# Kernel optimization log

Measured on AMD Instinct MI355X. Metric: run time of the kernel, lower is better.

The kernel has to match this reference:

```python
import jax, jax.numpy as jnp
import numpy as np

NUM_NEIGHBORS = 3
EPS = 1e-10
B, N1, N2 = 8, 8192, 2048
C1, C2 = 256, 512


def setup_inputs() -> dict:
    key = jax.random.key(0)
    k1, k2, k3, k4 = jax.random.split(key, 4)
    return {
        "query_xyz": jax.random.uniform(k1, (B, 3, N1), dtype=jnp.float32),
        "key_xyz": jax.random.uniform(k2, (B, 3, N2), dtype=jnp.float32),
        "query_feature": jax.random.normal(k3, (B, C1, N1), dtype=jnp.float32),
        "key_feature": jax.random.normal(k4, (B, C2, N2), dtype=jnp.float32),
    }


def reference(query_xyz, key_xyz, query_feature, key_feature):
    # q: (B, N1, 3), k: (B, N2, 3)
    q = jnp.swapaxes(query_xyz, 1, 2)
    k = jnp.swapaxes(key_xyz, 1, 2)
    # squared pairwise distances (B, N1, N2) via ||q||^2 + ||k||^2 - 2 q.k
    d2 = (
        jnp.sum(q * q, axis=-1, keepdims=True)
        + jnp.sum(k * k, axis=-1)[:, None, :]
        - 2.0 * jnp.einsum("bnd,bmd->bnm", q, k)
    )
    # k nearest neighbors (smallest distances)
    neg_d, index = jax.lax.top_k(-d2, NUM_NEIGHBORS)  # (B, N1, K)
    distance = jnp.maximum(-neg_d, EPS)
    inv_distance = 1.0 / distance
    weight = inv_distance / jnp.sum(inv_distance, axis=2, keepdims=True)
    # torch.no_grad() block -> constants w.r.t. autodiff
    weight = jax.lax.stop_gradient(weight)
    index = jax.lax.stop_gradient(index)
    # gather key features: feat_t (B, N2, C2) -> gathered (B, N1, K, C2)
    feat_t = jnp.swapaxes(key_feature, 1, 2)
    batch_idx = jnp.arange(feat_t.shape[0])[:, None, None]
    gathered = feat_t[batch_idx, index]
    # inverse-distance weighted sum -> (B, C2, N1)
    interpolated = jnp.einsum("bnk,bnkc->bcn", weight, gathered)
    return jnp.concatenate([interpolated, query_feature], axis=1)
```

## Files before the change

kernel.cpp:

```cpp
#include <hip/hip_runtime.h>

#define NB 8
#define N1 8192
#define N2 2048
#define C1 256
#define C2 512
#define CO 768
#define CCH 4


#define NRM2(X, Y, Z) ({                                                   \
    float _s, _t;                                                          \
    asm("v_mul_f32 %0, %2, %2\n\t"                                         \
        "v_mul_f32 %1, %3, %3\n\t"                                         \
        "v_add_f32 %0, %0, %1\n\t"                                         \
        "v_mul_f32 %1, %4, %4\n\t"                                         \
        "v_add_f32 %0, %0, %1"                                             \
        : "=&v"(_s), "=&v"(_t) : "v"(X), "v"(Y), "v"(Z));                  \
    _s; })

#define D2PIN(QX, QY, QZ, QQ, X, Y, Z, KK) ({                              \
    float _d, _t;                                                          \
    asm("v_mul_f32 %0, %2, %5\n\t"             \
        "v_fma_f32 %0, %3, %6, %0\n\t"         \
        "v_fma_f32 %0, %4, %7, %0\n\t"         \
        "v_add_f32 %1, %8, %9\n\t"             \
        "v_mul_f32 %0, 2.0, %0\n\t"            \
        "v_sub_f32 %0, %1, %0"                 \
        : "=&v"(_d), "=&v"(_t)                                             \
        : "v"(QX), "v"(QY), "v"(QZ), "v"(X), "v"(Y), "v"(Z),               \
          "v"(QQ), "v"(KK));                                               \
    _d; })

__global__ __launch_bounds__(256, 4) void knn_fused(
    const float* __restrict__ qxyz,
    const float* __restrict__ kxyz,
    int*   __restrict__ nn_idx,
    float* __restrict__ nn_w)
{
    __shared__ __align__(16) float skx[N2];
    __shared__ __align__(16) float sky[N2];
    __shared__ __align__(16) float skz[N2];
    __shared__ __align__(16) float skk[N2];
    __shared__ float pd[4][64][3];
    __shared__ int   pi[4][64][3];

    const int b   = blockIdx.x >> 7;
    const int n0  = (blockIdx.x & 127) * 64;
    const int tid = threadIdx.x;
    const int w   = tid >> 6, lane = tid & 63;

    const float* kb = kxyz + (size_t)b * 3 * N2;
    for (int j = tid; j < N2; j += 256) {
        float x = kb[j], y = kb[N2 + j], z = kb[2 * N2 + j];
        skx[j] = x; sky[j] = y; skz[j] = z;
        skk[j] = NRM2(x, y, z);
    }
    __syncthreads();

    const int n = n0 + lane;
    const float* qb = qxyz + (size_t)b * 3 * N1;
    const float qx = qb[n], qy = qb[N1 + n], qz = qb[2 * N1 + n];
    const float qq = NRM2(qx, qy, qz);

    float b0 = 3.4e38f, b1 = 3.4e38f, b2 = 3.4e38f;
    int   i0 = 0, i1 = 0, i2 = 0;

#define PROC(X, Y, Z, KK, J) do {                                          \
        float d2 = D2PIN(qx, qy, qz, qq, (X), (Y), (Z), (KK));             \
        if (d2 < b2) {                                                     \
            bool c0 = d2 < b0, c1 = d2 < b1;                               \
            b2 = c1 ? b1 : d2;               i2 = c1 ? i1 : (J);           \
            b1 = c0 ? b0 : (c1 ? d2 : b1);   i1 = c0 ? i0 : (c1 ? (J) : i1); \
            b0 = c0 ? d2 : b0;               i0 = c0 ? (J) : i0;           \
        }                                                                  \
    } while (0)

    const int jlo = w * (N2 / 4), jhi = jlo + (N2 / 4);
    #pragma unroll 4
    for (int jb = jlo; jb < jhi; jb += 4) {
        float4 x4 = *(const float4*)&skx[jb];
        float4 y4 = *(const float4*)&sky[jb];
        float4 z4 = *(const float4*)&skz[jb];
        float4 k4 = *(const float4*)&skk[jb];
        PROC(x4.x, y4.x, z4.x, k4.x, jb + 0);
        PROC(x4.y, y4.y, z4.y, k4.y, jb + 1);
        PROC(x4.z, y4.z, z4.z, k4.z, jb + 2);
        PROC(x4.w, y4.w, z4.w, k4.w, jb + 3);
    }
#undef PROC

    pd[w][lane][0] = b0; pd[w][lane][1] = b1; pd[w][lane][2] = b2;
    pi[w][lane][0] = i0; pi[w][lane][1] = i1; pi[w][lane][2] = i2;
    __syncthreads();

    if (tid < 64) {
        float m0 = 3.4e38f, m1 = 3.4e38f, m2 = 3.4e38f;
        int   j0 = 0, j1 = 0, j2 = 0;
        #pragma unroll
        for (int c = 0; c < 4; ++c) {
            #pragma unroll
            for (int s = 0; s < 3; ++s) {
                float d = pd[c][tid][s];
                int   i = pi[c][tid][s];
                if (d < m2) {
                    bool c0 = d < m0, c1 = d < m1;
                    m2 = c1 ? m1 : d;                j2 = c1 ? j1 : i;
                    m1 = c0 ? m0 : (c1 ? d : m1);    j1 = c0 ? j0 : (c1 ? i : j1);
                    m0 = c0 ? d : m0;                j0 = c0 ? i  : j0;
                }
            }
        }
        float d0f = fmaxf(m0, 1e-10f), d1f = fmaxf(m1, 1e-10f), d2f = fmaxf(m2, 1e-10f);
        float v0 = __fdiv_rn(1.0f, d0f), v1 = __fdiv_rn(1.0f, d1f), v2 = __fdiv_rn(1.0f, d2f);
        float s  = __fadd_rn(__fadd_rn(v0, v1), v2);
        const size_t p = ((size_t)b * N1 + n0 + tid) * 3;
        nn_idx[p] = j0; nn_idx[p + 1] = j1; nn_idx[p + 2] = j2;
        nn_w[p]   = __fdiv_rn(v0, s);
        nn_w[p+1] = __fdiv_rn(v1, s);
        nn_w[p+2] = __fdiv_rn(v2, s);
    }
}

__global__ __launch_bounds__(256) void interp3(
    const float* __restrict__ kfeat,
    const int*   __restrict__ nn_idx,
    const float* __restrict__ nn_w,
    float* __restrict__ out)
{
    __shared__ float skf[N2 * 5];
    const int b     = blockIdx.x & 7;
    const int cg    = blockIdx.x >> 3;
    const int cbase = cg * CCH;
    const int tid   = threadIdx.x;

    const float* kf = kfeat + (size_t)b * C2 * N2 + (size_t)cbase * N2;
    for (int idx = tid; idx < CCH * N2; idx += 256) {
        int c = idx >> 11, j = idx & (N2 - 1);
        skf[j * 5 + c] = kf[(size_t)c * N2 + j];
    }
    __syncthreads();

    const int*   ib = nn_idx + (size_t)b * N1 * 3;
    const float* wb = nn_w   + (size_t)b * N1 * 3;
    float* ob = out + (size_t)b * CO * N1;

    #pragma unroll 4
    for (int t = 0; t < N1 / 256; ++t) {
        const int n = t * 256 + tid;
        const int   i0 = ib[n * 3], i1 = ib[n * 3 + 1], i2 = ib[n * 3 + 2];
        const float w0 = wb[n * 3], w1 = wb[n * 3 + 1], w2 = wb[n * 3 + 2];
        #pragma unroll
        for (int c = 0; c < CCH; ++c) {
            float f0 = skf[i0 * 5 + c], f1 = skf[i1 * 5 + c], f2 = skf[i2 * 5 + c];
            ob[(size_t)(cbase + c) * N1 + n] =
                fmaf(w2, f2, fmaf(w1, f1, __fmul_rn(w0, f0)));
        }
    }
}

__global__ __launch_bounds__(256) void copy_kernel(
    const float* __restrict__ qfeat,
    float* __restrict__ out)
{
    const int b = blockIdx.x >> 11;
    const size_t r = ((size_t)(blockIdx.x & 2047)) * 256 + threadIdx.x;
    const float4* src = (const float4*)(qfeat + (size_t)b * C1 * N1);
    float4* dst = (float4*)(out + (size_t)b * CO * N1 + (size_t)C2 * N1);
    dst[r] = src[r];
}

extern "C" void kernel_launch(void* const* d_in, const int* in_sizes, int n_in,
                              void* d_out, int out_size, void* d_ws, size_t ws_size,
                              hipStream_t stream) {
    const float* qxyz  = (const float*)d_in[0];
    const float* kxyz  = (const float*)d_in[1];
    const float* qfeat = (const float*)d_in[2];
    const float* kfeat = (const float*)d_in[3];
    float* out = (float*)d_out;

    int*   nn_idx = (int*)d_ws;
    float* nn_w   = (float*)d_ws + (size_t)3 * NB * N1;

    knn_fused<<<NB * (N1 / 64), 256, 0, stream>>>(qxyz, kxyz, nn_idx, nn_w);
    interp3<<<NB * (C2 / CCH), 256, 0, stream>>>(kfeat, nn_idx, nn_w, out);
    copy_kernel<<<NB * 2048, 256, 0, stream>>>(qfeat, out);
}
```

Baseline: 113.5 us.

## Pad neighbor records to vec4, use float4 feature tiles, fuse copy into interp

Neighbor indices and weights are stored padded to four entries, so each point's record is read with a single 128-bit load. The four channels of each key point now sit together as one float4 in shared memory, so a gathered neighbor needs one LDS read instead of four scalar reads. The separate query-feature copy kernel is removed and its work is spread across the interpolation blocks, which saves a launch and lets the copy traffic overlap the gather. The trade-off is more workspace (4 entries per point instead of 3) and a heavier interpolation kernel.

```diff
diff --git a/kernel.cpp b/kernel.cpp
--- a/kernel.cpp
+++ b/kernel.cpp
@@ -114,60 +114,63 @@
         float d0f = fmaxf(m0, 1e-10f), d1f = fmaxf(m1, 1e-10f), d2f = fmaxf(m2, 1e-10f);
         float v0 = __fdiv_rn(1.0f, d0f), v1 = __fdiv_rn(1.0f, d1f), v2 = __fdiv_rn(1.0f, d2f);
         float s  = __fadd_rn(__fadd_rn(v0, v1), v2);
-        const size_t p = ((size_t)b * N1 + n0 + tid) * 3;
-        nn_idx[p] = j0; nn_idx[p + 1] = j1; nn_idx[p + 2] = j2;
-        nn_w[p]   = __fdiv_rn(v0, s);
-        nn_w[p+1] = __fdiv_rn(v1, s);
-        nn_w[p+2] = __fdiv_rn(v2, s);
+        const size_t g = (size_t)b * N1 + n0 + tid;
+        int4   iv = make_int4(j0, j1, j2, 0);
+        float4 wv = make_float4(__fdiv_rn(v0, s), __fdiv_rn(v1, s),
+                                __fdiv_rn(v2, s), 0.0f);
+        *(int4*)  &nn_idx[g * 4] = iv;
+        *(float4*)&nn_w  [g * 4] = wv;
     }
 }
 
-__global__ __launch_bounds__(256) void interp3(
+__global__ __launch_bounds__(256) void interp4(
     const float* __restrict__ kfeat,
     const int*   __restrict__ nn_idx,
     const float* __restrict__ nn_w,
+    const float* __restrict__ qfeat,
     float* __restrict__ out)
 {
-    __shared__ float skf[N2 * 5];
+    __shared__ __align__(16) float4 skf[N2];
     const int b     = blockIdx.x & 7;
     const int cg    = blockIdx.x >> 3;
     const int cbase = cg * CCH;
     const int tid   = threadIdx.x;
 
     const float* kf = kfeat + (size_t)b * C2 * N2 + (size_t)cbase * N2;
-    for (int idx = tid; idx < CCH * N2; idx += 256) {
-        int c = idx >> 11, j = idx & (N2 - 1);
-        skf[j * 5 + c] = kf[(size_t)c * N2 + j];
+    for (int j = tid; j < N2; j += 256) {
+        skf[j] = make_float4(kf[j], kf[N2 + j], kf[2 * N2 + j], kf[3 * N2 + j]);
     }
     __syncthreads();
 
-    const int*   ib = nn_idx + (size_t)b * N1 * 3;
-    const float* wb = nn_w   + (size_t)b * N1 * 3;
+    const int*   ib = nn_idx + (size_t)b * N1 * 4;
+    const float* wb = nn_w   + (size_t)b * N1 * 4;
     float* ob = out + (size_t)b * CO * N1;
 
     #pragma unroll 4
     for (int t = 0; t < N1 / 256; ++t) {
         const int n = t * 256 + tid;
-        const int   i0 = ib[n * 3], i1 = ib[n * 3 + 1], i2 = ib[n * 3 + 2];
-        const float w0 = wb[n * 3], w1 = wb[n * 3 + 1], w2 = wb[n * 3 + 2];
-        #pragma unroll
-        for (int c = 0; c < CCH; ++c) {
-            float f0 = skf[i0 * 5 + c], f1 = skf[i1 * 5 + c], f2 = skf[i2 * 5 + c];
-            ob[(size_t)(cbase + c) * N1 + n] =
-                fmaf(w2, f2, fmaf(w1, f1, __fmul_rn(w0, f0)));
-        }
+        const int4   iv = *(const int4*)  &ib[(size_t)n * 4];
+        const float4 wv = *(const float4*)&wb[(size_t)n * 4];
+        const float4 f0 = skf[iv.x];
+        const float4 f1 = skf[iv.y];
+        const float4 f2 = skf[iv.z];
+        ob[(size_t)(cbase + 0) * N1 + n] =
+            fmaf(wv.z, f2.x, fmaf(wv.y, f1.x, __fmul_rn(wv.x, f0.x)));
+        ob[(size_t)(cbase + 1) * N1 + n] =
+            fmaf(wv.z, f2.y, fmaf(wv.y, f1.y, __fmul_rn(wv.x, f0.y)));
+        ob[(size_t)(cbase + 2) * N1 + n] =
+            fmaf(wv.z, f2.z, fmaf(wv.y, f1.z, __fmul_rn(wv.x, f0.z)));
+        ob[(size_t)(cbase + 3) * N1 + n] =
+            fmaf(wv.z, f2.w, fmaf(wv.y, f1.w, __fmul_rn(wv.x, f0.w)));
     }
-}
 
-__global__ __launch_bounds__(256) void copy_kernel(
-    const float* __restrict__ qfeat,
-    float* __restrict__ out)
-{
-    const int b = blockIdx.x >> 11;
-    const size_t r = ((size_t)(blockIdx.x & 2047)) * 256 + threadIdx.x;
-    const float4* src = (const float4*)(qfeat + (size_t)b * C1 * N1);
-    float4* dst = (float4*)(out + (size_t)b * CO * N1 + (size_t)C2 * N1);
-    dst[r] = src[r];
+    const float4* qsrc = (const float4*)(qfeat + (size_t)b * C1 * N1);
+    float4*       qdst = (float4*)(out + (size_t)b * CO * N1 + (size_t)C2 * N1);
+    #pragma unroll
+    for (int k = 0; k < 16; ++k) {
+        const size_t r = (size_t)cg * 4096 + (size_t)k * 256 + tid;
+        qdst[r] = qsrc[r];
+    }
 }
 
 extern "C" void kernel_launch(void* const* d_in, const int* in_sizes, int n_in,
@@ -180,9 +183,8 @@
     float* out = (float*)d_out;
 
     int*   nn_idx = (int*)d_ws;
-    float* nn_w   = (float*)d_ws + (size_t)3 * NB * N1;
+    float* nn_w   = (float*)d_ws + (size_t)4 * NB * N1;
 
     knn_fused<<<NB * (N1 / 64), 256, 0, stream>>>(qxyz, kxyz, nn_idx, nn_w);
-    interp3<<<NB * (C2 / CCH), 256, 0, stream>>>(kfeat, nn_idx, nn_w, out);
-    copy_kernel<<<NB * 2048, 256, 0, stream>>>(qfeat, out);
+    interp4<<<NB * (C2 / CCH), 256, 0, stream>>>(kfeat, nn_idx, nn_w, qfeat, out);
 }
```

After: 116.0 us. 1.02x slower.
